# Kernel optimization log

Hardware: AMD Instinct MI355X
Metric: run time of the kernel (lower is better)

Reference implementation:

```python
import jax, jax.numpy as jnp
import numpy as np

N, E, F_IN, H, EA = 50000, 400000, 16, 128, 8


def _lin(k, fi, fo):
    return jax.random.normal(k, (fi, fo), jnp.float32) / np.float32(np.sqrt(fi))


def setup_inputs() -> dict:
    key = jax.random.key(0)
    ks = jax.random.split(key, 12)
    return {
        "x": jax.random.normal(ks[0], (N, F_IN), jnp.float32),
        "edge_index": jax.random.randint(ks[1], (2, E), 0, N, dtype=jnp.int64),
        "edge_attr": jax.random.normal(ks[2], (E, EA), jnp.float32),
        "layer_num": 3,
        "W_enc": _lin(ks[3], F_IN, H), "b_enc": jnp.zeros((H,), jnp.float32),
        "W_msg": _lin(ks[4], 2 * H, H), "b_msg": jnp.zeros((H,), jnp.float32),
        "W_upd": _lin(ks[5], 2 * H, H), "b_upd": jnp.zeros((H,), jnp.float32),
        "Wn1": _lin(ks[6], H, 64), "bn1": jnp.zeros((64,), jnp.float32),
        "Wn2": _lin(ks[7], 64, 2), "bn2": jnp.zeros((2,), jnp.float32),
        "We1": _lin(ks[8], 2 * H + EA, 128), "be1": jnp.zeros((128,), jnp.float32),
        "We2": _lin(ks[9], 128, 64), "be2": jnp.zeros((64,), jnp.float32),
        "We3": _lin(ks[10], 64, 6), "be3": jnp.zeros((6,), jnp.float32),
    }


def reference(x, edge_index, edge_attr, layer_num,
              W_enc, b_enc, W_msg, b_msg, W_upd, b_upd,
              Wn1, bn1, Wn2, bn2, We1, be1, We2, be2, We3, be3):
    n = x.shape[0]
    src, dst = edge_index[0], edge_index[1]
    # encoder: single linear (MLP with no hidden layers, no act)
    h = x @ W_enc + b_enc  # [N, H]
    # mean-aggregation degree (computed once; edge structure is static)
    deg = jax.ops.segment_sum(jnp.ones((src.shape[0], 1), h.dtype), dst,
                              num_segments=n)
    deg = jnp.maximum(deg, 1.0)
    # repeated graph-network layer + relu (gnn_act=True, dropout_p=0 -> no-op)
    for _ in range(layer_num):
        m = jnp.concatenate([h[src], h[dst]], axis=-1) @ W_msg + b_msg  # [E, H]
        agg = jax.ops.segment_sum(m, dst, num_segments=n) / deg          # [N, H]
        h = jnp.concatenate([h, agg], axis=-1) @ W_upd + b_upd           # [N, H]
        h = jax.nn.relu(h)
    # node head: Linear(H,64)-ReLU-Linear(64,2)
    node_out = jax.nn.relu(h @ Wn1 + bn1) @ Wn2 + bn2
    # edge head: gather src/dst embeddings, concat edge_attr, 3-layer MLP
    ef = jnp.concatenate([h[src], h[dst], edge_attr], axis=-1)  # [E, 2H+EA]
    edge_out = jax.nn.relu(jax.nn.relu(ef @ We1 + be1) @ We2 + be2) @ We3 + be3
    return (node_out, edge_out)
```

## Files before the change

### kernel.cpp

```cpp
#include <hip/hip_runtime.h>
#include <hip/hip_bf16.h>

#define HD 128

typedef __attribute__((ext_vector_type(8))) short bf16x8;
typedef __attribute__((ext_vector_type(4))) float f32x4;

__device__ __forceinline__ ushort f2bf(float f) {
    uint u = __float_as_uint(f);
    return (ushort)((u + 0x7FFFu + ((u >> 16) & 1u)) >> 16);
}
__device__ __forceinline__ float bf2f(ushort h) {
    return __uint_as_float(((uint)h) << 16);
}

__global__ __launch_bounds__(256) void encoder_kernel(
    const float* __restrict__ x, const float* __restrict__ W,
    const float* __restrict__ b, float* __restrict__ h, int N)
{
    int n = blockIdx.x * 2 + (threadIdx.x >> 7);
    int c = threadIdx.x & 127;
    if (n >= N) return;
    const float* xr = x + (size_t)n * 16;
    float acc = b[c];
#pragma unroll
    for (int k = 0; k < 16; ++k)
        acc = fmaf(xr[k], W[k * HD + c], acc);
    h[(size_t)n * HD + c] = acc;
}

__global__ __launch_bounds__(256) void deg_int_kernel(
    const int* __restrict__ dst, int* __restrict__ deg, int E)
{
    int e = blockIdx.x * 256 + threadIdx.x;
    if (e < E) atomicAdd(&deg[dst[e]], 1);
}

__global__ __launch_bounds__(256) void degscale_kernel(
    const int* __restrict__ deg, float* __restrict__ r,
    float* __restrict__ s, int N)
{
    int n = blockIdx.x * 256 + threadIdx.x;
    if (n < N) {
        float c = (float)deg[n];
        float cp = fmaxf(c, 1.0f);
        r[n] = 1.0f / cp;
        s[n] = c / cp;
    }
}

__global__ __launch_bounds__(256) void scan_kernel(
    const int* __restrict__ deg, int* __restrict__ off, int N)
{
    __shared__ int wsum[4];
    const int tid = threadIdx.x;
    const int lane = tid & 63;
    const int wid = tid >> 6;
    int carry = 0;
    for (int base = 0; base < N; base += 256) {
        int i = base + tid;
        int v = (i < N) ? deg[i] : 0;
        int x = v;
#pragma unroll
        for (int d = 1; d < 64; d <<= 1) {
            int y = __shfl_up(x, d);
            if (lane >= d) x += y;
        }
        if (lane == 63) wsum[wid] = x;
        __syncthreads();
        int add = 0;
#pragma unroll
        for (int w = 0; w < 3; ++w)
            if (w < wid) add += wsum[w];
        if (i < N) off[i] = carry + add + x - v;
        carry += wsum[0] + wsum[1] + wsum[2] + wsum[3];
        __syncthreads();
    }
    if (tid == 0) off[N] = carry;
}

__global__ __launch_bounds__(256) void csr_fill_kernel(
    const int* __restrict__ src, const int* __restrict__ dst,
    const int* __restrict__ off, int* __restrict__ cursor,
    int* __restrict__ csr_src, int* __restrict__ csr_dst,
    int* __restrict__ csr_eid, int E)
{
    int e = blockIdx.x * 256 + threadIdx.x;
    if (e < E) {
        int d = dst[e];
        int p = atomicAdd(&cursor[d], 1);
        int pos = off[d] + p;
        csr_src[pos] = src[e];
        csr_dst[pos] = d;
        csr_eid[pos] = e;
    }
}

__global__ __launch_bounds__(256) void pull_kernel(
    const float* __restrict__ h, const int* __restrict__ off,
    const int* __restrict__ csr, const float* __restrict__ r,
    float* __restrict__ S, int N)
{
    int n = blockIdx.x * 4 + (threadIdx.x >> 6);
    if (n >= N) return;
    int lane = threadIdx.x & 63;
    int beg = off[n], end = off[n + 1];
    float ax = 0.0f, ay = 0.0f;
    for (int i = beg; i < end; ++i) {
        int s = csr[i];
        float2 v = *reinterpret_cast<const float2*>(h + (size_t)s * HD + 2 * lane);
        ax += v.x; ay += v.y;
    }
    float rr = r[n];
    *reinterpret_cast<float2*>(S + (size_t)n * HD + 2 * lane) =
        make_float2(ax * rr, ay * rr);
}

__global__ __launch_bounds__(256) void wt_convert_kernel(
    const float* __restrict__ W, ushort* __restrict__ WThi,
    ushort* __restrict__ WTlo, int K, int C)
{
    int idx = blockIdx.x * 256 + threadIdx.x;
    if (idx >= K * C) return;
    int k = idx / C, c = idx % C;
    float a = W[idx];
    ushort hi = f2bf(a);
    ushort lo = f2bf(a - bf2f(hi));
    WThi[c * K + k] = hi;
    WTlo[c * K + k] = lo;
}

__global__ __launch_bounds__(256) void gemm_mfma_kernel(
    const float* __restrict__ A0, const float* __restrict__ A1,
    const float* __restrict__ s1,
    const ushort* __restrict__ WT_hi, const ushort* __restrict__ WT_lo,
    int wstride, int kw0,
    const float* __restrict__ bias, const float* __restrict__ bscale,
    float* __restrict__ out, int N, int K, int relu)
{
    __shared__ __align__(16) ushort Ahi_s[64][40];
    __shared__ __align__(16) ushort Alo_s[64][40];
    __shared__ __align__(16) ushort Bhi_s[128][40];
    __shared__ __align__(16) ushort Blo_s[128][40];

    const int tid    = threadIdx.x;
    const int n_base = blockIdx.x * 64;
    const int sa_row = tid >> 2;
    const int sa_k4  = (tid & 3) * 4;
    const int sa_ng  = min(n_base + sa_row, N - 1);
    const float scA1 = s1 ? s1[sa_ng] : 1.0f;
    const int sb_c = tid & 127;
    const int sb_h = (tid >> 7) * 16;
    const int lane = tid & 63, wv = tid >> 6;
    const int fr = lane & 15;
    const int fk = (lane >> 4) * 8;

    f32x4 acc[8];
#pragma unroll
    for (int t = 0; t < 8; ++t) acc[t] = (f32x4){0.f, 0.f, 0.f, 0.f};

    const int nsteps = K >> 5;
    for (int s = 0; s < nsteps; ++s) {
        const int k0 = s * 32;
        __syncthreads();
        const float* Ab; int kof; float sc;
        if (K == 256 && k0 >= 128) { Ab = A1; kof = k0 - 128; sc = scA1; }
        else                       { Ab = A0; kof = k0;       sc = 1.0f; }
#pragma unroll
        for (int ch = 0; ch < 32; ch += 16) {
            float4 v = *reinterpret_cast<const float4*>(
                Ab + (size_t)sa_ng * HD + kof + ch + sa_k4);
            float vv[4] = {v.x * sc, v.y * sc, v.z * sc, v.w * sc};
            ushort4 hi, lo;
            hi.x = f2bf(vv[0]); lo.x = f2bf(vv[0] - bf2f(hi.x));
            hi.y = f2bf(vv[1]); lo.y = f2bf(vv[1] - bf2f(hi.y));
            hi.z = f2bf(vv[2]); lo.z = f2bf(vv[2] - bf2f(hi.z));
            hi.w = f2bf(vv[3]); lo.w = f2bf(vv[3] - bf2f(hi.w));
            *reinterpret_cast<ushort4*>(&Ahi_s[sa_row][ch + sa_k4]) = hi;
            *reinterpret_cast<ushort4*>(&Alo_s[sa_row][ch + sa_k4]) = lo;
        }
        {
            const ushort* ph = WT_hi + (size_t)sb_c * wstride + kw0 + k0 + sb_h;
            const ushort* pl = WT_lo + (size_t)sb_c * wstride + kw0 + k0 + sb_h;
            *reinterpret_cast<uint4*>(&Bhi_s[sb_c][sb_h])     = *reinterpret_cast<const uint4*>(ph);
            *reinterpret_cast<uint4*>(&Bhi_s[sb_c][sb_h + 8]) = *reinterpret_cast<const uint4*>(ph + 8);
            *reinterpret_cast<uint4*>(&Blo_s[sb_c][sb_h])     = *reinterpret_cast<const uint4*>(pl);
            *reinterpret_cast<uint4*>(&Blo_s[sb_c][sb_h + 8]) = *reinterpret_cast<const uint4*>(pl + 8);
        }
        __syncthreads();
        bf16x8 ah = *reinterpret_cast<bf16x8*>(&Ahi_s[wv * 16 + fr][fk]);
        bf16x8 al = *reinterpret_cast<bf16x8*>(&Alo_s[wv * 16 + fr][fk]);
#pragma unroll
        for (int t = 0; t < 8; ++t) {
            bf16x8 bh = *reinterpret_cast<bf16x8*>(&Bhi_s[t * 16 + fr][fk]);
            bf16x8 bl = *reinterpret_cast<bf16x8*>(&Blo_s[t * 16 + fr][fk]);
            acc[t] = __builtin_amdgcn_mfma_f32_16x16x32_bf16(ah, bh, acc[t], 0, 0, 0);
            acc[t] = __builtin_amdgcn_mfma_f32_16x16x32_bf16(al, bh, acc[t], 0, 0, 0);
            acc[t] = __builtin_amdgcn_mfma_f32_16x16x32_bf16(ah, bl, acc[t], 0, 0, 0);
        }
    }
#pragma unroll
    for (int reg = 0; reg < 4; ++reg) {
        int n = n_base + wv * 16 + (lane >> 4) * 4 + reg;
        if (n < N) {
            float bs = bscale ? bscale[n] : 1.0f;
#pragma unroll
            for (int t = 0; t < 8; ++t) {
                int c = t * 16 + fr;
                float v = acc[t][reg] + (bias ? bias[c] * bs : 0.0f);
                out[(size_t)n * HD + c] = relu ? fmaxf(v, 0.0f) : v;
            }
        }
    }
}

__global__ __launch_bounds__(256) void node_head_kernel(
    const float* __restrict__ h,
    const float* __restrict__ W1, const float* __restrict__ b1,
    const float* __restrict__ W2, const float* __restrict__ b2,
    float* __restrict__ out, int N)
{
    int n = blockIdx.x * 4 + (threadIdx.x >> 6);
    int lane = threadIdx.x & 63;
    if (n >= N) return;
    const float* hr = h + (size_t)n * HD;
    float t = b1[lane];
#pragma unroll 16
    for (int k = 0; k < HD; ++k)
        t = fmaf(hr[k], W1[k * 64 + lane], t);
    t = fmaxf(t, 0.0f);
    float o0 = t * W2[lane * 2 + 0];
    float o1 = t * W2[lane * 2 + 1];
#pragma unroll
    for (int sft = 32; sft > 0; sft >>= 1) {
        o0 += __shfl_xor(o0, sft);
        o1 += __shfl_xor(o1, sft);
    }
    if (lane == 0) {
        out[(size_t)n * 2 + 0] = o0 + b2[0];
        out[(size_t)n * 2 + 1] = o1 + b2[1];
    }
}

__global__ __launch_bounds__(256) void edge_head_kernel(
    const float* __restrict__ P, const float* __restrict__ Q,
    const int* __restrict__ csr_src, const int* __restrict__ csr_dst,
    const int* __restrict__ csr_eid,
    const float* __restrict__ ea,
    const float* __restrict__ W1c, const float* __restrict__ b1,
    const ushort* __restrict__ W2Th, const ushort* __restrict__ W2Tl,
    const float* __restrict__ b2,
    const float* __restrict__ W3, const float* __restrict__ b3,
    float* __restrict__ out, int E)
{
    const int tid  = threadIdx.x;
    const int base = blockIdx.x * 64;
    const int lane = tid & 63, wv = tid >> 6;
    const int fr = lane & 15;
    const int hi16 = lane >> 4;
    const int fk = hi16 * 8;

    const int slot = min(base + wv * 16 + fr, E - 1);
    const int sn  = csr_src[slot];
    const int dn  = csr_dst[slot];
    const int eid = csr_eid[slot];

    float eav[8];
    {
        float4 e0 = *reinterpret_cast<const float4*>(ea + (size_t)eid * 8);
        float4 e1 = *reinterpret_cast<const float4*>(ea + (size_t)eid * 8 + 4);
        eav[0] = e0.x; eav[1] = e0.y; eav[2] = e0.z; eav[3] = e0.w;
        eav[4] = e1.x; eav[5] = e1.y; eav[6] = e1.z; eav[7] = e1.w;
    }

    bf16x8 ah[4], al[4];
#pragma unroll
    for (int kt = 0; kt < 4; ++kt) {
        const int c0 = kt * 32 + fk;
        float4 p0 = *reinterpret_cast<const float4*>(P + (size_t)sn * HD + c0);
        float4 p1 = *reinterpret_cast<const float4*>(P + (size_t)sn * HD + c0 + 4);
        float4 q0 = *reinterpret_cast<const float4*>(Q + (size_t)dn * HD + c0);
        float4 q1 = *reinterpret_cast<const float4*>(Q + (size_t)dn * HD + c0 + 4);
        float4 b0 = *reinterpret_cast<const float4*>(b1 + c0);
        float4 b1v = *reinterpret_cast<const float4*>(b1 + c0 + 4);
        float v[8];
        v[0] = p0.x + q0.x + b0.x;  v[1] = p0.y + q0.y + b0.y;
        v[2] = p0.z + q0.z + b0.z;  v[3] = p0.w + q0.w + b0.w;
        v[4] = p1.x + q1.x + b1v.x; v[5] = p1.y + q1.y + b1v.y;
        v[6] = p1.z + q1.z + b1v.z; v[7] = p1.w + q1.w + b1v.w;
#pragma unroll
        for (int k = 0; k < 8; ++k) {
            float4 w0 = *reinterpret_cast<const float4*>(W1c + k * HD + c0);
            float4 w1 = *reinterpret_cast<const float4*>(W1c + k * HD + c0 + 4);
            v[0] = fmaf(eav[k], w0.x, v[0]); v[1] = fmaf(eav[k], w0.y, v[1]);
            v[2] = fmaf(eav[k], w0.z, v[2]); v[3] = fmaf(eav[k], w0.w, v[3]);
            v[4] = fmaf(eav[k], w1.x, v[4]); v[5] = fmaf(eav[k], w1.y, v[5]);
            v[6] = fmaf(eav[k], w1.z, v[6]); v[7] = fmaf(eav[k], w1.w, v[7]);
        }
#pragma unroll
        for (int j = 0; j < 8; ++j) {
            float t = fmaxf(v[j], 0.0f);
            ushort h = f2bf(t);
            ushort l = f2bf(t - bf2f(h));
            ah[kt][j] = (short)h;
            al[kt][j] = (short)l;
        }
    }

    f32x4 acc[4];
#pragma unroll
    for (int t = 0; t < 4; ++t) acc[t] = (f32x4){0.f, 0.f, 0.f, 0.f};
#pragma unroll
    for (int kt = 0; kt < 4; ++kt) {
#pragma unroll
        for (int t = 0; t < 4; ++t) {
            const size_t boff = (size_t)(t * 16 + fr) * 128 + kt * 32 + fk;
            bf16x8 bh = *reinterpret_cast<const bf16x8*>(W2Th + boff);
            bf16x8 bl = *reinterpret_cast<const bf16x8*>(W2Tl + boff);
            acc[t] = __builtin_amdgcn_mfma_f32_16x16x32_bf16(ah[kt], bh, acc[t], 0, 0, 0);
            acc[t] = __builtin_amdgcn_mfma_f32_16x16x32_bf16(al[kt], bh, acc[t], 0, 0, 0);
            acc[t] = __builtin_amdgcn_mfma_f32_16x16x32_bf16(ah[kt], bl, acc[t], 0, 0, 0);
        }
    }

    float b2v[4];
#pragma unroll
    for (int t = 0; t < 4; ++t) b2v[t] = b2[t * 16 + fr];
#pragma unroll
    for (int reg = 0; reg < 4; ++reg) {
        int erow = wv * 16 + hi16 * 4 + reg;
        float p[6];
#pragma unroll
        for (int j = 0; j < 6; ++j) p[j] = 0.0f;
#pragma unroll
        for (int t = 0; t < 4; ++t) {
            int c = t * 16 + fr;
            float t2v = fmaxf(acc[t][reg] + b2v[t], 0.0f);
#pragma unroll
            for (int j = 0; j < 6; ++j)
                p[j] = fmaf(t2v, W3[c * 6 + j], p[j]);
        }
#pragma unroll
        for (int j = 0; j < 6; ++j) {
#pragma unroll
            for (int sft = 1; sft < 16; sft <<= 1)
                p[j] += __shfl_xor(p[j], sft);
        }
        int oslot = base + erow;
        if (fr < 6 && oslot < E) {
            int oeid = csr_eid[oslot];
            out[(size_t)oeid * 6 + fr] = p[fr] + b3[fr];
        }
    }
}

extern "C" void kernel_launch(void* const* d_in, const int* in_sizes, int n_in,
                              void* d_out, int out_size, void* d_ws, size_t ws_size,
                              hipStream_t stream)
{
    (void)n_in; (void)out_size; (void)ws_size;
    const float* x     = (const float*)d_in[0];
    const int*   ei    = (const int*)d_in[1];
    const float* eattr = (const float*)d_in[2];
    const float* Wenc = (const float*)d_in[4];
    const float* benc = (const float*)d_in[5];
    const float* Wmsg = (const float*)d_in[6];
    const float* bmsg = (const float*)d_in[7];
    const float* Wupd = (const float*)d_in[8];
    const float* bupd = (const float*)d_in[9];
    const float* Wn1  = (const float*)d_in[10];
    const float* bn1  = (const float*)d_in[11];
    const float* Wn2  = (const float*)d_in[12];
    const float* bn2  = (const float*)d_in[13];
    const float* We1  = (const float*)d_in[14];
    const float* be1  = (const float*)d_in[15];
    const float* We2  = (const float*)d_in[16];
    const float* be2  = (const float*)d_in[17];
    const float* We3  = (const float*)d_in[18];
    const float* be3  = (const float*)d_in[19];

    const int N = in_sizes[0] / 16;
    const int E = in_sizes[1] / 2;
    const int* src = ei;
    const int* dst = ei + E;

    float* h0   = (float*)d_ws;
    float* h1   = h0 + (size_t)N * HD;
    float* S    = h1 + (size_t)N * HD;
    float* agg  = S  + (size_t)N * HD;
    float* rs   = agg + (size_t)N * HD;
    float* ss   = rs + N;
    int* deg_i  = (int*)(ss + N);
    int* off    = deg_i + N;
    int* cursor = off + N + 1;
    int* csr_s  = cursor + N;
    int* csr_d  = csr_s + E;
    int* csr_e  = csr_d + E;
    ushort* wt  = (ushort*)(((uintptr_t)(csr_e + E) + 255) & ~(uintptr_t)255);
    ushort* wtm_hi = wt;
    ushort* wtm_lo = wtm_hi + 32768;
    ushort* wtu_hi = wtm_lo + 32768;
    ushort* wtu_lo = wtu_hi + 32768;
    ushort* wte_hi = wtu_lo + 32768;
    ushort* wte_lo = wte_hi + 32768;
    ushort* w2t_hi = wte_lo + 32768;
    ushort* w2t_lo = w2t_hi + 8192;

    float* node_out = (float*)d_out;
    float* edge_out = node_out + (size_t)N * 2;

    hipMemsetAsync(deg_i, 0, (size_t)N * sizeof(int), stream);
    hipMemsetAsync(cursor, 0, (size_t)N * sizeof(int), stream);
    deg_int_kernel<<<(E + 255) / 256, 256, 0, stream>>>(dst, deg_i, E);
    scan_kernel<<<1, 256, 0, stream>>>(deg_i, off, N);
    degscale_kernel<<<(N + 255) / 256, 256, 0, stream>>>(deg_i, rs, ss, N);
    csr_fill_kernel<<<(E + 255) / 256, 256, 0, stream>>>(
        src, dst, off, cursor, csr_s, csr_d, csr_e, E);

    wt_convert_kernel<<<128, 256, 0, stream>>>(Wmsg, wtm_hi, wtm_lo, 256, 128);
    wt_convert_kernel<<<128, 256, 0, stream>>>(Wupd, wtu_hi, wtu_lo, 256, 128);
    wt_convert_kernel<<<128, 256, 0, stream>>>(We1,  wte_hi, wte_lo, 256, 128);
    wt_convert_kernel<<<32,  256, 0, stream>>>(We2,  w2t_hi, w2t_lo, 128, 64);

    encoder_kernel<<<(N + 1) / 2, 256, 0, stream>>>(x, Wenc, benc, h0, N);

    const int gblocks = (N + 63) / 64;
    float* hc = h0;
    float* hn = h1;
    for (int l = 0; l < 3; ++l) {
        pull_kernel<<<(N + 3) / 4, 256, 0, stream>>>(hc, off, csr_s, rs, S, N);
        gemm_mfma_kernel<<<gblocks, 256, 0, stream>>>(
            S, hc, ss, wtm_hi, wtm_lo, 256, 0, bmsg, ss, agg, N, 256, 0);
        gemm_mfma_kernel<<<gblocks, 256, 0, stream>>>(
            hc, agg, nullptr, wtu_hi, wtu_lo, 256, 0, bupd, nullptr, hn, N, 256, 1);
        float* t = hc; hc = hn; hn = t;
    }

    float* Pb = S;
    float* Qb = agg;
    gemm_mfma_kernel<<<gblocks, 256, 0, stream>>>(
        hc, nullptr, nullptr, wte_hi, wte_lo, 256, 0, nullptr, nullptr, Pb, N, 128, 0);
    gemm_mfma_kernel<<<gblocks, 256, 0, stream>>>(
        hc, nullptr, nullptr, wte_hi, wte_lo, 256, 128, nullptr, nullptr, Qb, N, 128, 0);

    node_head_kernel<<<(N + 3) / 4, 256, 0, stream>>>(
        hc, Wn1, bn1, Wn2, bn2, node_out, N);
    edge_head_kernel<<<(E + 63) / 64, 256, 0, stream>>>(
        Pb, Qb, csr_s, csr_d, csr_e, eattr, We1 + (size_t)256 * HD, be1,
        w2t_hi, w2t_lo, be2, We3, be3, edge_out, E);
}
```

Measured before the change: 977.0 us.

## Fold message GEMM into update weights and stage edge-head gathers in LDS

Precomputes Wmsg·Wupd_bottom and bmsg·Wupd_bottom once, so each layer runs one K=384 GEMM over [h, S, ss*h] instead of two K=256 GEMMs with an agg round-trip through memory. The edge head is also restructured: node indices and edge attributes are staged in shared memory, and P/Q rows are gathered with coalesced per-wave float2 loads into an LDS tile before the MFMA work. The fold removes one GEMM launch and a full N×128 write and read per layer. In exchange the weight product is reassociated, which changes rounding slightly, and the edge head uses more shared memory.

New measurement: 942.8 us. 3.5% less time.

```diff
diff --git a/kernel.cpp b/kernel.cpp
--- a/kernel.cpp
+++ b/kernel.cpp
@@ -116,6 +116,48 @@
         make_float2(ax * rr, ay * rr);
 }
 
+__global__ __launch_bounds__(128) void mm2_kernel(
+    const float* __restrict__ Wmsg, const float* __restrict__ Wupd,
+    float* __restrict__ M)
+{
+    int b = blockIdx.x;
+    int j = threadIdx.x;
+    const float* Ar = Wmsg + (size_t)b * 128;
+    const float* B  = Wupd + 128 * 128;
+    float acc = 0.0f;
+#pragma unroll 8
+    for (int k = 0; k < 128; ++k)
+        acc = fmaf(Ar[k], B[k * 128 + j], acc);
+    M[(size_t)b * 128 + j] = acc;
+}
+
+__global__ __launch_bounds__(128) void cvec_kernel(
+    const float* __restrict__ bmsg, const float* __restrict__ Wupd,
+    float* __restrict__ cvec)
+{
+    int j = threadIdx.x;
+    const float* B = Wupd + 128 * 128;
+    float acc = 0.0f;
+#pragma unroll 8
+    for (int k = 0; k < 128; ++k)
+        acc = fmaf(bmsg[k], B[k * 128 + j], acc);
+    cvec[j] = acc;
+}
+
+__global__ __launch_bounds__(256) void wft_build_kernel(
+    const float* __restrict__ Wupd, const float* __restrict__ M12,
+    ushort* __restrict__ WThi, ushort* __restrict__ WTlo)
+{
+    int idx = blockIdx.x * 256 + threadIdx.x;
+    if (idx >= 384 * 128) return;
+    int k = idx >> 7, c = idx & 127;
+    float a = (k < 128) ? Wupd[idx] : M12[(size_t)(k - 128) * 128 + c];
+    ushort hi = f2bf(a);
+    ushort lo = f2bf(a - bf2f(hi));
+    WThi[(size_t)c * 384 + k] = hi;
+    WTlo[(size_t)c * 384 + k] = lo;
+}
+
 __global__ __launch_bounds__(256) void wt_convert_kernel(
     const float* __restrict__ W, ushort* __restrict__ WThi,
     ushort* __restrict__ WTlo, int K, int C)
@@ -128,6 +170,89 @@
     ushort lo = f2bf(a - bf2f(hi));
     WThi[c * K + k] = hi;
     WTlo[c * K + k] = lo;
+}
+
+__global__ __launch_bounds__(256) void gemm_fused_kernel(
+    const float* __restrict__ h, const float* __restrict__ S,
+    const float* __restrict__ ss,
+    const ushort* __restrict__ WT_hi, const ushort* __restrict__ WT_lo,
+    const float* __restrict__ bupd, const float* __restrict__ cvec,
+    float* __restrict__ out, int N)
+{
+    __shared__ __align__(16) ushort Ahi_s[64][40];
+    __shared__ __align__(16) ushort Alo_s[64][40];
+    __shared__ __align__(16) ushort Bhi_s[128][40];
+    __shared__ __align__(16) ushort Blo_s[128][40];
+
+    const int tid    = threadIdx.x;
+    const int n_base = blockIdx.x * 64;
+    const int sa_row = tid >> 2;
+    const int sa_k4  = (tid & 3) * 4;
+    const int sa_ng  = min(n_base + sa_row, N - 1);
+    const float scA  = ss[sa_ng];
+    const int sb_c = tid & 127;
+    const int sb_h = (tid >> 7) * 16;
+    const int lane = tid & 63, wv = tid >> 6;
+    const int fr = lane & 15;
+    const int fk = (lane >> 4) * 8;
+
+    f32x4 acc[8];
+#pragma unroll
+    for (int t = 0; t < 8; ++t) acc[t] = (f32x4){0.f, 0.f, 0.f, 0.f};
+
+    for (int s = 0; s < 12; ++s) {
+        const int k0 = s * 32;
+        __syncthreads();
+        const int part = k0 >> 7;
+        const int kof  = k0 & 127;
+        const float* Ab = (part == 1) ? S : h;
+        const float  sc = (part == 2) ? scA : 1.0f;
+#pragma unroll
+        for (int ch = 0; ch < 32; ch += 16) {
+            float4 v = *reinterpret_cast<const float4*>(
+                Ab + (size_t)sa_ng * HD + kof + ch + sa_k4);
+            float vv[4] = {v.x * sc, v.y * sc, v.z * sc, v.w * sc};
+            ushort4 hi, lo;
+            hi.x = f2bf(vv[0]); lo.x = f2bf(vv[0] - bf2f(hi.x));
+            hi.y = f2bf(vv[1]); lo.y = f2bf(vv[1] - bf2f(hi.y));
+            hi.z = f2bf(vv[2]); lo.z = f2bf(vv[2] - bf2f(hi.z));
+            hi.w = f2bf(vv[3]); lo.w = f2bf(vv[3] - bf2f(hi.w));
+            *reinterpret_cast<ushort4*>(&Ahi_s[sa_row][ch + sa_k4]) = hi;
+            *reinterpret_cast<ushort4*>(&Alo_s[sa_row][ch + sa_k4]) = lo;
+        }
+        {
+            const ushort* ph = WT_hi + (size_t)sb_c * 384 + k0 + sb_h;
+            const ushort* pl = WT_lo + (size_t)sb_c * 384 + k0 + sb_h;
+            *reinterpret_cast<uint4*>(&Bhi_s[sb_c][sb_h])     = *reinterpret_cast<const uint4*>(ph);
+            *reinterpret_cast<uint4*>(&Bhi_s[sb_c][sb_h + 8]) = *reinterpret_cast<const uint4*>(ph + 8);
+            *reinterpret_cast<uint4*>(&Blo_s[sb_c][sb_h])     = *reinterpret_cast<const uint4*>(pl);
+            *reinterpret_cast<uint4*>(&Blo_s[sb_c][sb_h + 8]) = *reinterpret_cast<const uint4*>(pl + 8);
+        }
+        __syncthreads();
+        bf16x8 ah = *reinterpret_cast<bf16x8*>(&Ahi_s[wv * 16 + fr][fk]);
+        bf16x8 al = *reinterpret_cast<bf16x8*>(&Alo_s[wv * 16 + fr][fk]);
+#pragma unroll
+        for (int t = 0; t < 8; ++t) {
+            bf16x8 bh = *reinterpret_cast<bf16x8*>(&Bhi_s[t * 16 + fr][fk]);
+            bf16x8 bl = *reinterpret_cast<bf16x8*>(&Blo_s[t * 16 + fr][fk]);
+            acc[t] = __builtin_amdgcn_mfma_f32_16x16x32_bf16(ah, bh, acc[t], 0, 0, 0);
+            acc[t] = __builtin_amdgcn_mfma_f32_16x16x32_bf16(al, bh, acc[t], 0, 0, 0);
+            acc[t] = __builtin_amdgcn_mfma_f32_16x16x32_bf16(ah, bl, acc[t], 0, 0, 0);
+        }
+    }
+#pragma unroll
+    for (int reg = 0; reg < 4; ++reg) {
+        int n = n_base + wv * 16 + (lane >> 4) * 4 + reg;
+        if (n < N) {
+            float sv = ss[n];
+#pragma unroll
+            for (int t = 0; t < 8; ++t) {
+                int c = t * 16 + fr;
+                float v = acc[t][reg] + bupd[c] + sv * cvec[c];
+                out[(size_t)n * HD + c] = fmaxf(v, 0.0f);
+            }
+        }
+    }
 }
 
 __global__ __launch_bounds__(256) void gemm_mfma_kernel(
@@ -253,41 +378,61 @@
     const float* __restrict__ W3, const float* __restrict__ b3,
     float* __restrict__ out, int E)
 {
+    __shared__ float t1pre[64][132];
+    __shared__ float ea_s[64][8];
+    __shared__ int sn_s[64], dn_s[64], eid_s[64];
+
     const int tid  = threadIdx.x;
     const int base = blockIdx.x * 64;
     const int lane = tid & 63, wv = tid >> 6;
-    const int fr = lane & 15;
-    const int hi16 = lane >> 4;
-    const int fk = hi16 * 8;
-
-    const int slot = min(base + wv * 16 + fr, E - 1);
-    const int sn  = csr_src[slot];
-    const int dn  = csr_dst[slot];
-    const int eid = csr_eid[slot];
-
+
+    if (tid < 64) {
+        int slot = min(base + tid, E - 1);
+        sn_s[tid]  = csr_src[slot];
+        dn_s[tid]  = csr_dst[slot];
+        eid_s[tid] = csr_eid[slot];
+    }
+    __syncthreads();
+
+    if (tid < 128) {
+        int e = tid >> 1, q = (tid & 1) * 4;
+        float4 v = *reinterpret_cast<const float4*>(ea + (size_t)eid_s[e] * 8 + q);
+        *reinterpret_cast<float4*>(&ea_s[e][q]) = v;
+    }
+
+    float2 b1v = *reinterpret_cast<const float2*>(b1 + 2 * lane);
+    float2 pv[16], qv[16];
+#pragma unroll
+    for (int i = 0; i < 16; ++i) {
+        int e = wv * 16 + i;
+        pv[i] = *reinterpret_cast<const float2*>(P + (size_t)sn_s[e] * HD + 2 * lane);
+    }
+#pragma unroll
+    for (int i = 0; i < 16; ++i) {
+        int e = wv * 16 + i;
+        qv[i] = *reinterpret_cast<const float2*>(Q + (size_t)dn_s[e] * HD + 2 * lane);
+    }
+#pragma unroll
+    for (int i = 0; i < 16; ++i) {
+        int e = wv * 16 + i;
+        t1pre[e][2 * lane]     = pv[i].x + qv[i].x + b1v.x;
+        t1pre[e][2 * lane + 1] = pv[i].y + qv[i].y + b1v.y;
+    }
+    __syncthreads();
+
+    const int fr = lane & 15, hi16 = lane >> 4, fk = hi16 * 8;
+    const int eL = wv * 16 + fr;
     float eav[8];
-    {
-        float4 e0 = *reinterpret_cast<const float4*>(ea + (size_t)eid * 8);
-        float4 e1 = *reinterpret_cast<const float4*>(ea + (size_t)eid * 8 + 4);
-        eav[0] = e0.x; eav[1] = e0.y; eav[2] = e0.z; eav[3] = e0.w;
-        eav[4] = e1.x; eav[5] = e1.y; eav[6] = e1.z; eav[7] = e1.w;
-    }
+#pragma unroll
+    for (int k = 0; k < 8; ++k) eav[k] = ea_s[eL][k];
 
     bf16x8 ah[4], al[4];
 #pragma unroll
     for (int kt = 0; kt < 4; ++kt) {
         const int c0 = kt * 32 + fk;
-        float4 p0 = *reinterpret_cast<const float4*>(P + (size_t)sn * HD + c0);
-        float4 p1 = *reinterpret_cast<const float4*>(P + (size_t)sn * HD + c0 + 4);
-        float4 q0 = *reinterpret_cast<const float4*>(Q + (size_t)dn * HD + c0);
-        float4 q1 = *reinterpret_cast<const float4*>(Q + (size_t)dn * HD + c0 + 4);
-        float4 b0 = *reinterpret_cast<const float4*>(b1 + c0);
-        float4 b1v = *reinterpret_cast<const float4*>(b1 + c0 + 4);
-        float v[8];
-        v[0] = p0.x + q0.x + b0.x;  v[1] = p0.y + q0.y + b0.y;
-        v[2] = p0.z + q0.z + b0.z;  v[3] = p0.w + q0.w + b0.w;
-        v[4] = p1.x + q1.x + b1v.x; v[5] = p1.y + q1.y + b1v.y;
-        v[6] = p1.z + q1.z + b1v.z; v[7] = p1.w + q1.w + b1v.w;
+        float4 v0 = *reinterpret_cast<float4*>(&t1pre[eL][c0]);
+        float4 v1 = *reinterpret_cast<float4*>(&t1pre[eL][c0 + 4]);
+        float v[8] = {v0.x, v0.y, v0.z, v0.w, v1.x, v1.y, v1.z, v1.w};
 #pragma unroll
         for (int k = 0; k < 8; ++k) {
             float4 w0 = *reinterpret_cast<const float4*>(W1c + k * HD + c0);
@@ -348,8 +493,7 @@
         }
         int oslot = base + erow;
         if (fr < 6 && oslot < E) {
-            int oeid = csr_eid[oslot];
-            out[(size_t)oeid * 6 + fr] = p[fr] + b3[fr];
+            out[(size_t)eid_s[erow] * 6 + fr] = p[fr] + b3[fr];
         }
     }
 }
@@ -387,8 +531,8 @@
     float* h0   = (float*)d_ws;
     float* h1   = h0 + (size_t)N * HD;
     float* S    = h1 + (size_t)N * HD;
-    float* agg  = S  + (size_t)N * HD;
-    float* rs   = agg + (size_t)N * HD;
+    float* Qb   = S  + (size_t)N * HD;
+    float* rs   = Qb + (size_t)N * HD;
     float* ss   = rs + N;
     int* deg_i  = (int*)(ss + N);
     int* off    = deg_i + N;
@@ -396,12 +540,13 @@
     int* csr_s  = cursor + N;
     int* csr_d  = csr_s + E;
     int* csr_e  = csr_d + E;
-    ushort* wt  = (ushort*)(((uintptr_t)(csr_e + E) + 255) & ~(uintptr_t)255);
-    ushort* wtm_hi = wt;
-    ushort* wtm_lo = wtm_hi + 32768;
-    ushort* wtu_hi = wtm_lo + 32768;
-    ushort* wtu_lo = wtu_hi + 32768;
-    ushort* wte_hi = wtu_lo + 32768;
+    float* fM   = (float*)(((uintptr_t)(csr_e + E) + 255) & ~(uintptr_t)255);
+    float* M12  = fM;
+    float* cvec = fM + 32768;
+    ushort* wt  = (ushort*)(cvec + 128);
+    ushort* wft_hi = wt;
+    ushort* wft_lo = wft_hi + 49152;
+    ushort* wte_hi = wft_lo + 49152;
     ushort* wte_lo = wte_hi + 32768;
     ushort* w2t_hi = wte_lo + 32768;
     ushort* w2t_lo = w2t_hi + 8192;
@@ -417,10 +562,11 @@
     csr_fill_kernel<<<(E + 255) / 256, 256, 0, stream>>>(
         src, dst, off, cursor, csr_s, csr_d, csr_e, E);
 
-    wt_convert_kernel<<<128, 256, 0, stream>>>(Wmsg, wtm_hi, wtm_lo, 256, 128);
-    wt_convert_kernel<<<128, 256, 0, stream>>>(Wupd, wtu_hi, wtu_lo, 256, 128);
-    wt_convert_kernel<<<128, 256, 0, stream>>>(We1,  wte_hi, wte_lo, 256, 128);
-    wt_convert_kernel<<<32,  256, 0, stream>>>(We2,  w2t_hi, w2t_lo, 128, 64);
+    mm2_kernel<<<256, 128, 0, stream>>>(Wmsg, Wupd, M12);
+    cvec_kernel<<<1, 128, 0, stream>>>(bmsg, Wupd, cvec);
+    wft_build_kernel<<<192, 256, 0, stream>>>(Wupd, M12, wft_hi, wft_lo);
+    wt_convert_kernel<<<128, 256, 0, stream>>>(We1, wte_hi, wte_lo, 256, 128);
+    wt_convert_kernel<<<32,  256, 0, stream>>>(We2, w2t_hi, w2t_lo, 128, 64);
 
     encoder_kernel<<<(N + 1) / 2, 256, 0, stream>>>(x, Wenc, benc, h0, N);
 
@@ -429,15 +575,12 @@
     float* hn = h1;
     for (int l = 0; l < 3; ++l) {
         pull_kernel<<<(N + 3) / 4, 256, 0, stream>>>(hc, off, csr_s, rs, S, N);
-        gemm_mfma_kernel<<<gblocks, 256, 0, stream>>>(
-            S, hc, ss, wtm_hi, wtm_lo, 256, 0, bmsg, ss, agg, N, 256, 0);
-        gemm_mfma_kernel<<<gblocks, 256, 0, stream>>>(
-            hc, agg, nullptr, wtu_hi, wtu_lo, 256, 0, bupd, nullptr, hn, N, 256, 1);
+        gemm_fused_kernel<<<gblocks, 256, 0, stream>>>(
+            hc, S, ss, wft_hi, wft_lo, bupd, cvec, hn, N);
         float* t = hc; hc = hn; hn = t;
     }
 
     float* Pb = S;
-    float* Qb = agg;
     gemm_mfma_kernel<<<gblocks, 256, 0, stream>>>(
         hc, nullptr, nullptr, wte_hi, wte_lo, 256, 0, nullptr, nullptr, Pb, N, 128, 0);
     gemm_mfma_kernel<<<gblocks, 256, 0, stream>>>(
```
